# Kernel optimization log

Measured on AMD Instinct MI355X. Metric: run time of the kernel, lower is better.

## Reference

```python
import jax, jax.numpy as jnp
import numpy as np

SPATIAL_SHAPES = [(100, 152), (50, 76), (25, 38), (13, 19)]
D_MODEL = 256
N_HEADS = 8
N_LEVELS = 4
N_POINTS = 4
D_FFN = 1024
D_HEAD = D_MODEL // N_HEADS
EPS = 1e-5


def layernorm(x, g, b):
    mu = jnp.mean(x, axis=-1, keepdims=True)
    var = jnp.var(x, axis=-1, keepdims=True)
    return (x - mu) * jax.lax.rsqrt(var + EPS) * g + b


def bilinear_sample(value_l, H, W, locs):
    # value_l: (N, H*W, nH, dH); locs: (N, Lq, nH, P, 2) normalized to [0,1]
    # Matches torch grid_sample(align_corners=False, padding_mode='zeros') with grid=2*loc-1.
    N, Lq = locs.shape[0], locs.shape[1]
    x = locs[..., 0] * W - 0.5  # (N, Lq, nH, P) pixel coords
    y = locs[..., 1] * H - 0.5
    x0 = jnp.floor(x)
    y0 = jnp.floor(y)
    fx = x - x0
    fy = y - y0
    x0 = x0.astype(jnp.int32)
    y0 = y0.astype(jnp.int32)
    out = jnp.zeros((N, Lq, N_POINTS, N_HEADS, D_HEAD), value_l.dtype)
    for dy in (0, 1):
        for dx in (0, 1):
            xi = x0 + dx
            yi = y0 + dy
            w = (fx if dx else 1.0 - fx) * (fy if dy else 1.0 - fy)
            valid = (xi >= 0) & (xi < W) & (yi >= 0) & (yi < H)
            idx = jnp.clip(yi, 0, H - 1) * W + jnp.clip(xi, 0, W - 1)  # (N, Lq, nH, P)
            idx = idx.transpose(0, 1, 3, 2).reshape(N, Lq * N_POINTS, N_HEADS, 1)
            g = jnp.take_along_axis(value_l, idx, axis=1)  # (N, Lq*P, nH, dH)
            g = g.reshape(N, Lq, N_POINTS, N_HEADS, D_HEAD)
            wv = jnp.where(valid, w, 0.0).transpose(0, 1, 3, 2)[..., None]  # (N, Lq, P, nH, 1)
            out = out + g * wv
    return out  # (N, Lq, P, nH, dH)


def msdeform_attn(query, value_in, ref_points,
                  w_value, b_value, w_off, b_off, w_attn, b_attn, w_out, b_out):
    N, Lq, _ = query.shape
    value = (value_in @ w_value + b_value).reshape(N, -1, N_HEADS, D_HEAD)
    off = (query @ w_off + b_off).reshape(N, Lq, N_HEADS, N_LEVELS, N_POINTS, 2)
    attn = (query @ w_attn + b_attn).reshape(N, Lq, N_HEADS, N_LEVELS * N_POINTS)
    attn = jax.nn.softmax(attn, axis=-1).reshape(N, Lq, N_HEADS, N_LEVELS, N_POINTS)
    # offset normalizer is (W, H) per level
    norm = jnp.array([[w, h] for (h, w) in SPATIAL_SHAPES], dtype=query.dtype)  # (L, 2)
    locs = ref_points[:, :, None, :, None, :] + off / norm[None, None, None, :, None, :]
    out = jnp.zeros((N, Lq, N_HEADS, D_HEAD), query.dtype)
    start = 0
    for l, (H, W) in enumerate(SPATIAL_SHAPES):
        v_l = value[:, start:start + H * W]
        s = bilinear_sample(v_l, H, W, locs[:, :, :, l])  # (N, Lq, P, nH, dH)
        out = out + jnp.einsum('nqhp,nqphd->nqhd', attn[:, :, :, l], s)
        start += H * W
    out = out.reshape(N, Lq, D_MODEL)
    return out @ w_out + b_out


def setup_inputs() -> dict:
    key = jax.random.key(0)
    ks = jax.random.split(key, 20)
    B = 2
    Lq = sum(h * w for h, w in SPATIAL_SHAPES)  # 20197
    scale = 0.02
    inp = {
        'src': jax.random.normal(ks[0], (B, Lq, D_MODEL), jnp.float32),
        'pos': jax.random.normal(ks[1], (B, Lq, D_MODEL), jnp.float32),
        'reference_points': jax.random.uniform(ks[2], (B, Lq, N_LEVELS, 2), jnp.float32),
        'spatial_shapes': jnp.array(SPATIAL_SHAPES, dtype=jnp.int32),
        'level_start_index': jnp.array(np.cumsum([0] + [h * w for h, w in SPATIAL_SHAPES[:-1]]), dtype=jnp.int32),
        'w_value': jax.random.normal(ks[3], (D_MODEL, D_MODEL), jnp.float32) * scale,
        'b_value': jnp.zeros((D_MODEL,), jnp.float32),
        'w_off': jax.random.normal(ks[4], (D_MODEL, N_HEADS * N_LEVELS * N_POINTS * 2), jnp.float32) * scale,
        'b_off': jax.random.normal(ks[5], (N_HEADS * N_LEVELS * N_POINTS * 2,), jnp.float32) * scale,
        'w_attn': jax.random.normal(ks[6], (D_MODEL, N_HEADS * N_LEVELS * N_POINTS), jnp.float32) * scale,
        'b_attn': jnp.zeros((N_HEADS * N_LEVELS * N_POINTS,), jnp.float32),
        'w_out': jax.random.normal(ks[7], (D_MODEL, D_MODEL), jnp.float32) * scale,
        'b_out': jnp.zeros((D_MODEL,), jnp.float32),
        'g1': jnp.ones((D_MODEL,), jnp.float32),
        'beta1': jnp.zeros((D_MODEL,), jnp.float32),
        'w1': jax.random.normal(ks[8], (D_MODEL, D_FFN), jnp.float32) * scale,
        'b1': jnp.zeros((D_FFN,), jnp.float32),
        'w2': jax.random.normal(ks[9], (D_FFN, D_MODEL), jnp.float32) * scale,
        'b2': jnp.zeros((D_MODEL,), jnp.float32),
        'g2': jnp.ones((D_MODEL,), jnp.float32),
        'beta2': jnp.zeros((D_MODEL,), jnp.float32),
    }
    return inp


def reference(src, pos, reference_points, spatial_shapes, level_start_index,
              w_value, b_value, w_off, b_off, w_attn, b_attn, w_out, b_out,
              g1, beta1, w1, b1, w2, b2, g2, beta2):
    query = src + pos
    src2 = msdeform_attn(query, src, reference_points,
                         w_value, b_value, w_off, b_off, w_attn, b_attn, w_out, b_out)
    src = layernorm(src + src2, g1, beta1)
    h = jax.nn.relu(src @ w1 + b1)
    src = layernorm(src + h @ w2 + b2, g2, beta2)
    return src
```

## Files before the change

kernel.cpp:

```cpp
#include <hip/hip_runtime.h>

#define LQ   20197
#define MTOT 40394

typedef _Float16 f16;
typedef _Float16 f16x8 __attribute__((ext_vector_type(8)));
typedef _Float16 f16x4 __attribute__((ext_vector_type(4)));
typedef _Float16 f16x2 __attribute__((ext_vector_type(2)));
typedef float    f32x4 __attribute__((ext_vector_type(4)));

#define OFF_WT 0ull
#define OFF_B4 1507328ull
#define OFF_B1 42870784ull
#define OFF_B2 63552512ull
#define OFF_B3 84234240ull
#define OFF_B5 104915968ull
#define OFF_B6 125597696ull

#define WT_V    0
#define WT_OFF  65536
#define WT_ATTN 131072
#define WT_OUT  163840
#define WT_W1   229376
#define WT_W2   491520
#define WT_TOTAL 753664
#define WCONV_TOTAL (WT_TOTAL + 384)

__device__ __forceinline__ void gload_lds16(const f16* g, f16* l) {
    __builtin_amdgcn_global_load_lds(
        (const __attribute__((address_space(1))) unsigned int*)g,
        (__attribute__((address_space(3))) unsigned int*)l,
        16, 0, 0);
}

__global__ __launch_bounds__(256) void k_wconv(
    const float* __restrict__ wv, const float* __restrict__ woff,
    const float* __restrict__ wattn, const float* __restrict__ wout,
    const float* __restrict__ w1, const float* __restrict__ w2,
    const float* __restrict__ boff, const float* __restrict__ battn,
    f16* __restrict__ dst, float* __restrict__ biasoa)
{
    int gid = blockIdx.x * 256 + threadIdx.x;
    if (gid >= WCONV_TOTAL) return;
    if (gid >= WT_TOTAL) {
        int i = gid - WT_TOTAL;
        biasoa[i] = (i < 256) ? boff[i] : battn[i - 256];
        return;
    }
    const float* src; int Kd, Nd, base;
    if      (gid < 65536)  { src = wv;    Kd = 256;  Nd = 256;  base = 0; }
    else if (gid < 131072) { src = woff;  Kd = 256;  Nd = 256;  base = 65536; }
    else if (gid < 163840) { src = wattn; Kd = 256;  Nd = 128;  base = 131072; }
    else if (gid < 229376) { src = wout;  Kd = 256;  Nd = 256;  base = 163840; }
    else if (gid < 491520) { src = w1;    Kd = 256;  Nd = 1024; base = 229376; }
    else                   { src = w2;    Kd = 1024; Nd = 256;  base = 491520; }
    int loc = gid - base;
    int n = loc % Nd, k = loc / Nd;
    dst[base + n * Kd + k] = (f16)src[k * Nd + n];
}

__global__ __launch_bounds__(256) void k_prep(
    const float* __restrict__ src, const float* __restrict__ pos,
    f16* __restrict__ srch, f16* __restrict__ qh, int total4)
{
    int i = blockIdx.x * 256 + threadIdx.x;
    if (i >= total4) return;
    float4 s = ((const float4*)src)[i];
    float4 p = ((const float4*)pos)[i];
    f16x4 hs = { (f16)s.x, (f16)s.y, (f16)s.z, (f16)s.w };
    f16x4 hq = { (f16)(s.x + p.x), (f16)(s.y + p.y), (f16)(s.z + p.z), (f16)(s.w + p.w) };
    ((f16x4*)srch)[i] = hs;
    ((f16x4*)qh)[i]   = hq;
}

template<bool RELU, int OUTM>
__global__ __launch_bounds__(256) void k_gemm128(
    const f16* __restrict__ A, const f16* __restrict__ Bt,
    const float* __restrict__ bias, void* __restrict__ Cout,
    int M, int N, int K)
{
    __shared__ __align__(16) char pool[34816];
    f16* const sm = (f16*)pool;

    const int NBn = N >> 7;
    const int MBn = (M + 127) >> 7;
    const int tiles = MBn * NBn;
    const int q = gridDim.x >> 3;
    const int bid = blockIdx.x;
    const int swz = (bid & 7) * q + (bid >> 3);
    if (swz >= tiles) return;
    const int m0 = (swz / NBn) << 7;
    const int n0 = (swz % NBn) << 7;

    const int t = threadIdx.x, wid = t >> 6, lane = t & 63;

    const int c0 = wid, c1 = wid + 4;
    const int sr = lane >> 2, sk = (lane & 3) * 8;
    const int ra0 = min(m0 + c0 * 16 + sr, M - 1);
    const int ra1 = min(m0 + c1 * 16 + sr, M - 1);
    const f16* pa0 = A + (size_t)ra0 * K + sk;
    const f16* pa1 = A + (size_t)ra1 * K + sk;
    const f16* pb0 = Bt + (size_t)(n0 + c0 * 16 + sr) * K + sk;
    const f16* pb1 = Bt + (size_t)(n0 + c1 * 16 + sr) * K + sk;
    const int lo0 = c0 * 512, lo1 = c1 * 512;

    const int wr = wid >> 1, wc = wid & 1;
    const int fr = lane & 15, kb = (lane >> 4) * 8;

    f32x4 acc[4][4] = {};
    const int NT = K >> 5;

    gload_lds16(pa0, sm + lo0);
    gload_lds16(pa1, sm + lo1);
    gload_lds16(pb0, sm + 4096 + lo0);
    gload_lds16(pb1, sm + 4096 + lo1);
    __syncthreads();

    for (int tt = 0; tt < NT; ++tt) {
        const int cur = (tt & 1) << 13, nxt = cur ^ 8192;
        if (tt + 1 < NT) {
            const int k0 = (tt + 1) << 5;
            gload_lds16(pa0 + k0, sm + nxt + lo0);
            gload_lds16(pa1 + k0, sm + nxt + lo1);
            gload_lds16(pb0 + k0, sm + nxt + 4096 + lo0);
            gload_lds16(pb1 + k0, sm + nxt + 4096 + lo1);
        }
        f16x8 af[4], bf[4];
#pragma unroll
        for (int i = 0; i < 4; ++i)
            af[i] = *(const f16x8*)&sm[cur + (wr * 64 + i * 16 + fr) * 32 + kb];
#pragma unroll
        for (int i = 0; i < 4; ++i)
            bf[i] = *(const f16x8*)&sm[cur + 4096 + (wc * 64 + i * 16 + fr) * 32 + kb];
#pragma unroll
        for (int mi = 0; mi < 4; ++mi)
#pragma unroll
            for (int ni = 0; ni < 4; ++ni)
                acc[mi][ni] = __builtin_amdgcn_mfma_f32_16x16x32_f16(af[mi], bf[ni], acc[mi][ni], 0, 0, 0);
        __syncthreads();
    }

    const int r4 = (lane >> 4) * 4;
#pragma unroll
    for (int ni = 0; ni < 4; ++ni) {
        const int lcol = wc * 64 + ni * 16 + fr;
        const float bv = bias[n0 + lcol];
#pragma unroll
        for (int mi = 0; mi < 4; ++mi) {
#pragma unroll
            for (int j = 0; j < 4; ++j) {
                float v = acc[mi][ni][j] + bv;
                if (RELU) v = fmaxf(v, 0.f);
                sm[(wr * 64 + mi * 16 + r4 + j) * 136 + lcol] = (f16)v;
            }
        }
    }
    __syncthreads();

    if (OUTM == 1) {
        const int rr = t >> 4, cc = (t & 15) * 8;
#pragma unroll
        for (int pass = 0; pass < 8; ++pass) {
            const int r = pass * 16 + rr;
            const int row = m0 + r;
            if (row < M) {
                f16x8 v = *(const f16x8*)&sm[r * 136 + cc];
                *(f16x8*)&((f16*)Cout)[(size_t)row * N + n0 + cc] = v;
            }
        }
    } else {
        const int cbl = t >> 6, rr = (t & 63) >> 2, cc = (t & 3) * 8;
        const size_t cb = (size_t)((n0 >> 5) + cbl);
#pragma unroll
        for (int pass = 0; pass < 8; ++pass) {
            const int r = pass * 16 + rr;
            const int row = m0 + r;
            if (row < M) {
                f16x8 v = *(const f16x8*)&sm[r * 136 + cbl * 32 + cc];
                *(f16x8*)&((f16*)Cout)[(cb * M + row) * 32 + cc] = v;
            }
        }
    }
}

__global__ __launch_bounds__(256) void k_sample(
    const f16* __restrict__ oa, const f16* __restrict__ valueT,
    const float* __restrict__ ref, f16* __restrict__ samp)
{
    __shared__ uint2 s_g[8][8][17];
    __shared__ f16x8 s_w[8][8][17];

    const int nblk = (MTOT + 7) / 8;
    const int q = gridDim.x >> 3;
    const int swz = (blockIdx.x & 7) * q + (blockIdx.x >> 3);
    if (swz >= nblk) return;
    const int tok0 = swz * 8;
    const int t = threadIdx.x;

#pragma unroll
    for (int it = 0; it < 4; ++it) {
        const int gid = it * 256 + t;
        const int tl = gid >> 7, h = (gid >> 4) & 7, lp = gid & 15, l = lp >> 2;
        const int tok = tok0 + tl;
        if (tok < MTOT) {
            const size_t row = (size_t)tok * 384;
            float logit = (float)oa[row + 256 + h * 16 + lp];
            float mx = logit;
#pragma unroll
            for (int m = 1; m < 16; m <<= 1) mx = fmaxf(mx, __shfl_xor(mx, m));
            float e = __expf(logit - mx);
            float sum = e;
#pragma unroll
            for (int m = 1; m < 16; m <<= 1) sum += __shfl_xor(sum, m);
            const float aw = e / sum;

            const float fW = (l == 0) ? 152.f : (l == 1) ? 76.f : (l == 2) ? 38.f : 19.f;
            const float fH = (l == 0) ? 100.f : (l == 1) ? 50.f : (l == 2) ? 25.f : 13.f;
            const int   W  = (l == 0) ? 152 : (l == 1) ? 76 : (l == 2) ? 38 : 19;
            const int   H  = (l == 0) ? 100 : (l == 1) ? 50 : (l == 2) ? 25 : 13;
            const int   st = (l == 0) ? 0 : (l == 1) ? 15200 : (l == 2) ? 19000 : 19950;

            const f16x2 ov = *(const f16x2*)&oa[row + h * 32 + lp * 2];
            const float2 rxy = *(const float2*)&ref[(size_t)tok * 8 + l * 2];
            const float x = rxy.x * fW + (float)ov.x - 0.5f;
            const float y = rxy.y * fH + (float)ov.y - 0.5f;
            const float xf = floorf(x), yf = floorf(y);
            const float fx = x - xf, fy = y - yf;
            const int x0 = (int)xf, y0 = (int)yf;

            const bool vx0 = (x0 >= 0) && (x0 < W);
            const bool vx1 = (x0 >= -1) && (x0 < W - 1);
            const bool vy0 = (y0 >= 0) && (y0 < H);
            const bool vy1 = (y0 >= -1) && (y0 < H - 1);
            const int x0c = min(max(x0, 0), W - 1), x1c = min(max(x0 + 1, 0), W - 1);
            const int y0c = min(max(y0, 0), H - 1), y1c = min(max(y0 + 1, 0), H - 1);

            const int n = (tok >= LQ) ? 1 : 0;
            const unsigned int b00 = ((unsigned int)(n * LQ + st + y0c * W + x0c) << 6)
                                   + (unsigned int)h * (MTOT * 64u);
            const unsigned int dx6 = (unsigned int)(x1c - x0c) << 6;
            const unsigned int dy6 = (unsigned int)((y1c - y0c) * W) << 6;
            s_g[tl][h][lp] = make_uint2(b00, dx6 | (dy6 << 16));

            const f16 w00 = (f16)((vx0 && vy0) ? (1.f - fx) * (1.f - fy) * aw : 0.f);
            const f16 w01 = (f16)((vx1 && vy0) ? fx * (1.f - fy) * aw : 0.f);
            const f16 w10 = (f16)((vx0 && vy1) ? (1.f - fx) * fy * aw : 0.f);
            const f16 w11 = (f16)((vx1 && vy1) ? fx * fy * aw : 0.f);
            f16x8 wv = { w00, w00, w01, w01, w10, w10, w11, w11 };
            s_w[tl][h][lp] = wv;
        }
    }
    __syncthreads();

    const int tl = t >> 5, h = (t >> 2) & 7, l4 = t & 3;
    const int tok = tok0 + tl;
    if (tok >= MTOT) return;
    const unsigned int lb = (unsigned int)l4 * 16u;
    const char* vbase = (const char*)valueT;

    f16x2 a0 = {}, a1 = {}, a2 = {}, a3 = {};
#pragma unroll 4
    for (int p = 0; p < 16; ++p) {
        const uint2 g  = s_g[tl][h][p];
        const f16x8 wv = s_w[tl][h][p];
        const unsigned int a00 = g.x + lb;
        const unsigned int dx6 = g.y & 0xFFFFu;
        const unsigned int dy6 = g.y >> 16;
        const f16x8 v00 = *(const f16x8*)(vbase + a00);
        const f16x8 v01 = *(const f16x8*)(vbase + (a00 + dx6));
        const f16x8 v10 = *(const f16x8*)(vbase + (a00 + dy6));
        const f16x8 v11 = *(const f16x8*)(vbase + (a00 + dy6 + dx6));
        const f16x2 w00 = { wv[0], wv[1] }, w01 = { wv[2], wv[3] };
        const f16x2 w10 = { wv[4], wv[5] }, w11 = { wv[6], wv[7] };
        const f16x2* p00 = (const f16x2*)&v00;
        const f16x2* p01 = (const f16x2*)&v01;
        const f16x2* p10 = (const f16x2*)&v10;
        const f16x2* p11 = (const f16x2*)&v11;
        a0 = a0 + p00[0] * w00; a1 = a1 + p00[1] * w00;
        a2 = a2 + p00[2] * w00; a3 = a3 + p00[3] * w00;
        a0 = a0 + p01[0] * w01; a1 = a1 + p01[1] * w01;
        a2 = a2 + p01[2] * w01; a3 = a3 + p01[3] * w01;
        a0 = a0 + p10[0] * w10; a1 = a1 + p10[1] * w10;
        a2 = a2 + p10[2] * w10; a3 = a3 + p10[3] * w10;
        a0 = a0 + p11[0] * w11; a1 = a1 + p11[1] * w11;
        a2 = a2 + p11[2] * w11; a3 = a3 + p11[3] * w11;
    }
    f16x8 o = { a0.x, a0.y, a1.x, a1.y, a2.x, a2.y, a3.x, a3.y };
    *(f16x8*)&samp[(size_t)tok * 256 + h * 32 + l4 * 8] = o;
}

__global__ __launch_bounds__(256) void k_ln1(
    const float* __restrict__ xa, const f16* __restrict__ xb,
    const float* __restrict__ g, const float* __restrict__ be,
    f16* __restrict__ yh, int M)
{
    const int row = blockIdx.x * 4 + (threadIdx.x >> 6);
    const int lane = threadIdx.x & 63;
    if (row >= M) return;
    const size_t o = (size_t)row * 256 + lane * 4;
    float4 a = *(const float4*)(xa + o);
    f16x4  b = *(const f16x4*)(xb + o);
    float x0 = a.x + (float)b.x, x1 = a.y + (float)b.y;
    float x2 = a.z + (float)b.z, x3 = a.w + (float)b.w;
    float s  = x0 + x1 + x2 + x3;
    float ss = x0*x0 + x1*x1 + x2*x2 + x3*x3;
#pragma unroll
    for (int m = 1; m < 64; m <<= 1) { s += __shfl_xor(s, m); ss += __shfl_xor(ss, m); }
    const float mean = s * (1.f / 256.f);
    const float var  = ss * (1.f / 256.f) - mean * mean;
    const float rstd = rsqrtf(var + 1e-5f);
    float4 gv = *(const float4*)(g + lane * 4);
    float4 bv = *(const float4*)(be + lane * 4);
    f16x4 hv = { (f16)((x0 - mean) * rstd * gv.x + bv.x),
                 (f16)((x1 - mean) * rstd * gv.y + bv.y),
                 (f16)((x2 - mean) * rstd * gv.z + bv.z),
                 (f16)((x3 - mean) * rstd * gv.w + bv.w) };
    *(f16x4*)(yh + o) = hv;
}

__global__ __launch_bounds__(256) void k_ln2(
    const f16* __restrict__ xa, const f16* __restrict__ xb,
    const float* __restrict__ g, const float* __restrict__ be,
    float* __restrict__ yf, int M)
{
    const int row = blockIdx.x * 4 + (threadIdx.x >> 6);
    const int lane = threadIdx.x & 63;
    if (row >= M) return;
    const size_t o = (size_t)row * 256 + lane * 4;
    f16x4 a = *(const f16x4*)(xa + o);
    f16x4 b = *(const f16x4*)(xb + o);
    float x0 = (float)a.x + (float)b.x, x1 = (float)a.y + (float)b.y;
    float x2 = (float)a.z + (float)b.z, x3 = (float)a.w + (float)b.w;
    float s  = x0 + x1 + x2 + x3;
    float ss = x0*x0 + x1*x1 + x2*x2 + x3*x3;
#pragma unroll
    for (int m = 1; m < 64; m <<= 1) { s += __shfl_xor(s, m); ss += __shfl_xor(ss, m); }
    const float mean = s * (1.f / 256.f);
    const float var  = ss * (1.f / 256.f) - mean * mean;
    const float rstd = rsqrtf(var + 1e-5f);
    float4 gv = *(const float4*)(g + lane * 4);
    float4 bv = *(const float4*)(be + lane * 4);
    float4 yo = { (x0 - mean) * rstd * gv.x + bv.x,
                  (x1 - mean) * rstd * gv.y + bv.y,
                  (x2 - mean) * rstd * gv.z + bv.z,
                  (x3 - mean) * rstd * gv.w + bv.w };
    *(float4*)(yf + o) = yo;
}

extern "C" void kernel_launch(void* const* d_in, const int* in_sizes, int n_in,
                              void* d_out, int out_size, void* d_ws, size_t ws_size,
                              hipStream_t stream) {
    const float* src   = (const float*)d_in[0];
    const float* pos   = (const float*)d_in[1];
    const float* ref   = (const float*)d_in[2];
    const float* w_value = (const float*)d_in[5];
    const float* b_value = (const float*)d_in[6];
    const float* w_off   = (const float*)d_in[7];
    const float* b_off   = (const float*)d_in[8];
    const float* w_attn  = (const float*)d_in[9];
    const float* b_attn  = (const float*)d_in[10];
    const float* w_out   = (const float*)d_in[11];
    const float* b_out   = (const float*)d_in[12];
    const float* g1    = (const float*)d_in[13];
    const float* beta1 = (const float*)d_in[14];
    const float* w1    = (const float*)d_in[15];
    const float* b1    = (const float*)d_in[16];
    const float* w2    = (const float*)d_in[17];
    const float* b2    = (const float*)d_in[18];
    const float* g2    = (const float*)d_in[19];
    const float* beta2 = (const float*)d_in[20];

    char* ws = (char*)d_ws;
    f16*   wT      = (f16*)(ws + OFF_WT);
    f16*   oa      = (f16*)(ws + OFF_B4);
    f16*   y2h     = (f16*)(ws + OFF_B4);
    f16*   srch    = (f16*)(ws + OFF_B1);
    f16*   samph   = (f16*)(ws + OFF_B1);
    f16*   qh      = (f16*)(ws + OFF_B2);
    f16*   x1h     = (f16*)(ws + OFF_B2);
    f16*   valueT  = (f16*)(ws + OFF_B3);
    f16*   hh      = (f16*)(ws + OFF_B3);
    float* biasoa  = (float*)(ws + OFF_B5);
    f16*   src2h   = (f16*)(ws + OFF_B6);
    float* outp    = (float*)d_out;

    const int M = MTOT;
    const int MB = (M + 127) / 128;
    auto grid8 = [&](int nb) { return ((MB * nb) + 7) & ~7; };

    k_wconv<<<(WCONV_TOTAL + 255) / 256, 256, 0, stream>>>(
        w_value, w_off, w_attn, w_out, w1, w2, b_off, b_attn, wT, biasoa);
    k_prep<<<(M * 64 + 255) / 256, 256, 0, stream>>>(src, pos, srch, qh, M * 64);

    k_gemm128<false, 2><<<grid8(2), 256, 0, stream>>>(srch, wT + WT_V, b_value, valueT, M, 256, 256);
    k_gemm128<false, 1><<<grid8(3), 256, 0, stream>>>(qh, wT + WT_OFF, biasoa, oa, M, 384, 256);
    {
        const int nblk = (MTOT + 7) / 8;
        const int g = (nblk + 7) & ~7;
        k_sample<<<dim3(g), 256, 0, stream>>>(oa, valueT, ref, samph);
    }
    k_gemm128<false, 1><<<grid8(2), 256, 0, stream>>>(samph, wT + WT_OUT, b_out, src2h, M, 256, 256);
    k_ln1<<<(M + 3) / 4, 256, 0, stream>>>(src, src2h, g1, beta1, x1h, M);
    k_gemm128<true, 1><<<grid8(8), 256, 0, stream>>>(x1h, wT + WT_W1, b1, hh, M, 1024, 256);
    k_gemm128<false, 1><<<grid8(2), 256, 0, stream>>>(hh, wT + WT_W2, b2, y2h, M, 256, 1024);
    k_ln2<<<(M + 3) / 4, 256, 0, stream>>>(x1h, y2h, g2, beta2, outp, M);

    (void)in_sizes; (void)n_in; (void)out_size; (void)ws_size;
}
```

Before: 237.1 us.

## Restructure deformable sampling blocks to one head per block over 64 tokens

Each sampling block now handles a single head for 64 tokens instead of all 8 heads for 8 tokens, with blockIdx low bits selecting the head. Consecutive blocks that share a token chunk thus read from different head planes of valueT. The intent is that blocks running together gather from one head plane, giving better cache locality. Sampling weights are stored as f16x4 instead of duplicated f16x8, which halves that shared-memory footprint. The old XCD-style block swizzle is removed, which may change how work spreads across chiplets' L2 caches.

```diff
diff --git a/kernel.cpp b/kernel.cpp
--- a/kernel.cpp
+++ b/kernel.cpp
@@ -187,24 +187,20 @@
     const f16* __restrict__ oa, const f16* __restrict__ valueT,
     const float* __restrict__ ref, f16* __restrict__ samp)
 {
-    __shared__ uint2 s_g[8][8][17];
-    __shared__ f16x8 s_w[8][8][17];
-
-    const int nblk = (MTOT + 7) / 8;
-    const int q = gridDim.x >> 3;
-    const int swz = (blockIdx.x & 7) * q + (blockIdx.x >> 3);
-    if (swz >= nblk) return;
-    const int tok0 = swz * 8;
+    __shared__ uint2 s_g[64][17];
+    __shared__ f16x4 s_w[64][17];
+    const int head = blockIdx.x & 7;
+    const int tok0 = (blockIdx.x >> 3) * 64;
     const int t = threadIdx.x;
 
 #pragma unroll
     for (int it = 0; it < 4; ++it) {
-        const int gid = it * 256 + t;
-        const int tl = gid >> 7, h = (gid >> 4) & 7, lp = gid & 15, l = lp >> 2;
+        const int tl = it * 16 + (t >> 4);
+        const int lp = t & 15, l = lp >> 2;
         const int tok = tok0 + tl;
         if (tok < MTOT) {
             const size_t row = (size_t)tok * 384;
-            float logit = (float)oa[row + 256 + h * 16 + lp];
+            float logit = (float)oa[row + 256 + head * 16 + lp];
             float mx = logit;
 #pragma unroll
             for (int m = 1; m < 16; m <<= 1) mx = fmaxf(mx, __shfl_xor(mx, m));
@@ -220,7 +216,7 @@
             const int   H  = (l == 0) ? 100 : (l == 1) ? 50 : (l == 2) ? 25 : 13;
             const int   st = (l == 0) ? 0 : (l == 1) ? 15200 : (l == 2) ? 19000 : 19950;
 
-            const f16x2 ov = *(const f16x2*)&oa[row + h * 32 + lp * 2];
+            const f16x2 ov = *(const f16x2*)&oa[row + head * 32 + lp * 2];
             const float2 rxy = *(const float2*)&ref[(size_t)tok * 8 + l * 2];
             const float x = rxy.x * fW + (float)ov.x - 0.5f;
             const float y = rxy.y * fH + (float)ov.y - 0.5f;
@@ -236,33 +232,32 @@
             const int y0c = min(max(y0, 0), H - 1), y1c = min(max(y0 + 1, 0), H - 1);
 
             const int n = (tok >= LQ) ? 1 : 0;
-            const unsigned int b00 = ((unsigned int)(n * LQ + st + y0c * W + x0c) << 6)
-                                   + (unsigned int)h * (MTOT * 64u);
+            const unsigned int b00 = (unsigned int)(n * LQ + st + y0c * W + x0c) << 6;
             const unsigned int dx6 = (unsigned int)(x1c - x0c) << 6;
             const unsigned int dy6 = (unsigned int)((y1c - y0c) * W) << 6;
-            s_g[tl][h][lp] = make_uint2(b00, dx6 | (dy6 << 16));
+            s_g[tl][lp] = make_uint2(b00, dx6 | (dy6 << 16));
 
             const f16 w00 = (f16)((vx0 && vy0) ? (1.f - fx) * (1.f - fy) * aw : 0.f);
             const f16 w01 = (f16)((vx1 && vy0) ? fx * (1.f - fy) * aw : 0.f);
             const f16 w10 = (f16)((vx0 && vy1) ? (1.f - fx) * fy * aw : 0.f);
             const f16 w11 = (f16)((vx1 && vy1) ? fx * fy * aw : 0.f);
-            f16x8 wv = { w00, w00, w01, w01, w10, w10, w11, w11 };
-            s_w[tl][h][lp] = wv;
+            f16x4 wv = { w00, w01, w10, w11 };
+            s_w[tl][lp] = wv;
         }
     }
     __syncthreads();
 
-    const int tl = t >> 5, h = (t >> 2) & 7, l4 = t & 3;
+    const int tl = t >> 2, l4 = t & 3;
     const int tok = tok0 + tl;
     if (tok >= MTOT) return;
     const unsigned int lb = (unsigned int)l4 * 16u;
-    const char* vbase = (const char*)valueT;
+    const char* vbase = (const char*)valueT + (size_t)head * (MTOT * 64ull);
 
     f16x2 a0 = {}, a1 = {}, a2 = {}, a3 = {};
 #pragma unroll 4
     for (int p = 0; p < 16; ++p) {
-        const uint2 g  = s_g[tl][h][p];
-        const f16x8 wv = s_w[tl][h][p];
+        const uint2 g  = s_g[tl][p];
+        const f16x4 wv = s_w[tl][p];
         const unsigned int a00 = g.x + lb;
         const unsigned int dx6 = g.y & 0xFFFFu;
         const unsigned int dy6 = g.y >> 16;
@@ -270,8 +265,8 @@
         const f16x8 v01 = *(const f16x8*)(vbase + (a00 + dx6));
         const f16x8 v10 = *(const f16x8*)(vbase + (a00 + dy6));
         const f16x8 v11 = *(const f16x8*)(vbase + (a00 + dy6 + dx6));
-        const f16x2 w00 = { wv[0], wv[1] }, w01 = { wv[2], wv[3] };
-        const f16x2 w10 = { wv[4], wv[5] }, w11 = { wv[6], wv[7] };
+        const f16x2 w00 = { wv[0], wv[0] }, w01 = { wv[1], wv[1] };
+        const f16x2 w10 = { wv[2], wv[2] }, w11 = { wv[3], wv[3] };
         const f16x2* p00 = (const f16x2*)&v00;
         const f16x2* p01 = (const f16x2*)&v01;
         const f16x2* p10 = (const f16x2*)&v10;
@@ -286,7 +281,7 @@
         a2 = a2 + p11[2] * w11; a3 = a3 + p11[3] * w11;
     }
     f16x8 o = { a0.x, a0.y, a1.x, a1.y, a2.x, a2.y, a3.x, a3.y };
-    *(f16x8*)&samp[(size_t)tok * 256 + h * 32 + l4 * 8] = o;
+    *(f16x8*)&samp[(size_t)tok * 256 + head * 32 + l4 * 8] = o;
 }
 
 __global__ __launch_bounds__(256) void k_ln1(
@@ -395,9 +390,8 @@
     k_gemm128<false, 2><<<grid8(2), 256, 0, stream>>>(srch, wT + WT_V, b_value, valueT, M, 256, 256);
     k_gemm128<false, 1><<<grid8(3), 256, 0, stream>>>(qh, wT + WT_OFF, biasoa, oa, M, 384, 256);
     {
-        const int nblk = (MTOT + 7) / 8;
-        const int g = (nblk + 7) & ~7;
-        k_sample<<<dim3(g), 256, 0, stream>>>(oa, valueT, ref, samph);
+        const int nchunk = (MTOT + 63) / 64;
+        k_sample<<<dim3(nchunk * 8), 256, 0, stream>>>(oa, valueT, ref, samph);
     }
     k_gemm128<false, 1><<<grid8(2), 256, 0, stream>>>(samph, wT + WT_OUT, b_out, src2h, M, 256, 256);
     k_ln1<<<(M + 3) / 4, 256, 0, stream>>>(src, src2h, g1, beta1, x1h, M);
```

New measurement: 222.5 us. 6.1% less time.
